# Kernel optimization log

Hardware: AMD Instinct MI355X
Metric: run time of the kernel (lower is better)

## Reference

```python
import jax, jax.numpy as jnp
import numpy as np

DIM = 1024
HEADS = 16
HEAD_DIM = DIM // HEADS
SCALE = HEAD_DIM ** -0.5
B, N = 2, 2048


def setup_inputs() -> dict:
    key = jax.random.key(0)
    ks = jax.random.split(key, 12)
    s = DIM ** -0.5
    return {
        "x_real": jax.random.normal(ks[0], (B, N, DIM), jnp.float32),
        "x_imag": jax.random.normal(ks[1], (B, N, DIM), jnp.float32),
        "Wqkv_r": jax.random.normal(ks[2], (3 * DIM, DIM), jnp.float32) * s,
        "bqkv_r": jax.random.normal(ks[3], (3 * DIM,), jnp.float32) * 0.01,
        "Wqkv_i": jax.random.normal(ks[4], (3 * DIM, DIM), jnp.float32) * s,
        "bqkv_i": jax.random.normal(ks[5], (3 * DIM,), jnp.float32) * 0.01,
        "Wout_r": jax.random.normal(ks[6], (DIM, DIM), jnp.float32) * s,
        "bout_r": jax.random.normal(ks[7], (DIM,), jnp.float32) * 0.01,
        "Wout_i": jax.random.normal(ks[8], (DIM, DIM), jnp.float32) * s,
        "bout_i": jax.random.normal(ks[9], (DIM,), jnp.float32) * 0.01,
    }


def _split_heads(qkv):
    # (B, N, 3*D) -> q, k, v each (B, H, N, hd)
    b, n, _ = qkv.shape
    qkv = qkv.reshape(b, n, 3, HEADS, HEAD_DIM).transpose(2, 0, 3, 1, 4)
    return qkv[0], qkv[1], qkv[2]


def reference(x_real, x_imag, Wqkv_r, bqkv_r, Wqkv_i, bqkv_i,
              Wout_r, bout_r, Wout_i, bout_i):
    b, n, d = x_real.shape
    q_r, k_r, v_r = _split_heads(x_real @ Wqkv_r.T + bqkv_r)
    q_i, k_i, v_i = _split_heads(x_imag @ Wqkv_i.T + bqkv_i)

    # complex score: (q_r + i q_i) (k_r - i k_i)^T pattern per source
    attn_real = (jnp.einsum('bhqd,bhkd->bhqk', q_r, k_r)
                 + jnp.einsum('bhqd,bhkd->bhqk', q_i, k_i)) * SCALE
    attn_imag = (jnp.einsum('bhqd,bhkd->bhqk', q_i, k_r)
                 - jnp.einsum('bhqd,bhkd->bhqk', q_r, k_i)) * SCALE
    attn_mag = jnp.sqrt(attn_real ** 2 + attn_imag ** 2)
    w = jax.nn.softmax(attn_mag, axis=-1)

    out_r = jnp.einsum('bhqk,bhkd->bhqd', w, v_r).transpose(0, 2, 1, 3).reshape(b, n, d)
    out_i = jnp.einsum('bhqk,bhkd->bhqd', w, v_i).transpose(0, 2, 1, 3).reshape(b, n, d)
    out_r = out_r @ Wout_r.T + bout_r
    out_i = out_i @ Wout_i.T + bout_i
    return out_r, out_i
```

## Files before the change

### kernel.cpp

```cpp
#include <hip/hip_runtime.h>


#define DIM_   1024
#define HEADS_ 16
#define HD_    64
#define BB_    2
#define NN_    2048
#define MTOT_  (BB_*NN_)
#define SCALE_ 0.125f
#define QSCALE_ 0.1803368801111243f

typedef __bf16 bf16;
typedef __bf16 bf16x8 __attribute__((ext_vector_type(8)));
typedef short  s16x8  __attribute__((ext_vector_type(8)));
typedef float  fx4    __attribute__((ext_vector_type(4)));

__device__ __forceinline__ bf16x8 neg8(bf16x8 v) {
    s16x8 s;
    __builtin_memcpy(&s, &v, sizeof(s));
    s ^= (short)0x8000;
    bf16x8 r;
    __builtin_memcpy(&r, &s, sizeof(r));
    return r;
}

__device__ __forceinline__ void gl_lds16(const void* g, void* l) {
    __builtin_amdgcn_global_load_lds(
        (const __attribute__((address_space(1))) unsigned int*)g,
        (__attribute__((address_space(3))) unsigned int*)l, 16, 0, 0);
}

#define PIPE_SYNC() asm volatile("s_waitcnt vmcnt(2)\n\ts_barrier" ::: "memory")
#define FULL_SYNC() asm volatile("s_waitcnt vmcnt(0)\n\ts_barrier" ::: "memory")

__global__ __launch_bounds__(256) void cvt_prepass(
    const float* __restrict__ xr, const float* __restrict__ xi,
    const float* __restrict__ wqr, const float* __restrict__ wqi,
    const float* __restrict__ wor, const float* __restrict__ woi,
    bf16* __restrict__ xbf, bf16* __restrict__ wqkv, bf16* __restrict__ wout)
{
    const int bid = blockIdx.x;
    const float* src; bf16* dst; int rel;
    if      (bid < 2048) { src = xr;  dst = xbf;           rel = bid; }
    else if (bid < 4096) { src = xi;  dst = xbf + 4194304; rel = bid - 2048; }
    else if (bid < 5632) { src = wqr; dst = wqkv;          rel = bid - 4096; }
    else if (bid < 7168) { src = wqi; dst = wqkv + 3145728; rel = bid - 5632; }
    else if (bid < 7680) { src = wor; dst = wout;          rel = bid - 7168; }
    else                 { src = woi; dst = wout + 1048576; rel = bid - 7680; }
    size_t base = (size_t)rel * 2048 + (size_t)threadIdx.x * 8;
    fx4 a = *(const fx4*)(src + base);
    fx4 b = *(const fx4*)(src + base + 4);
    bf16x8 o;
#pragma unroll
    for (int j = 0; j < 4; ++j) { o[j] = (bf16)a[j]; o[j+4] = (bf16)b[j]; }
    *(bf16x8*)(dst + base) = o;
}

#define GEMM_CORE(Aptr, Bptr)                                                  \
    __shared__ __align__(16) bf16 As[128*64];                                  \
    __shared__ __align__(16) bf16 Bs[128*64];                                  \
    const int tid  = threadIdx.x;                                              \
    const int w    = tid >> 6, lane = tid & 63;                                \
    const int quad = lane >> 4, lc = lane & 15;                                \
    const int wm   = (w >> 1) * 64, wn = (w & 1) * 64;                         \
    const int rj   = lane >> 3;                                                \
    const int sc   = (lane & 7) ^ rj;                                          \
    const fx4 fzero = {0.f, 0.f, 0.f, 0.f};                                    \
    fx4 acc[4][4];                                                             \
    _Pragma("unroll")                                                          \
    for (int mi = 0; mi < 4; ++mi)                                             \
        _Pragma("unroll")                                                      \
        for (int ni = 0; ni < 4; ++ni) acc[mi][ni] = fzero;                    \
    for (int k0 = 0; k0 < DIM_; k0 += 64) {                                    \
        _Pragma("unroll")                                                      \
        for (int j = 0; j < 4; ++j) {                                          \
            int grp = j*4 + w;                                                 \
            int gr  = grp*8 + rj;                                              \
            gl_lds16(Aptr + (size_t)(m0+gr)*DIM_ + k0 + sc*8, As + grp*512);   \
            gl_lds16(Bptr + (size_t)(n0+gr)*DIM_ + k0 + sc*8, Bs + grp*512);   \
        }                                                                      \
        __syncthreads();                                                       \
        bf16x8 af[2][4], bfr[2][4];                                            \
        _Pragma("unroll")                                                      \
        for (int ks = 0; ks < 2; ++ks) {                                       \
            _Pragma("unroll")                                                  \
            for (int mi = 0; mi < 4; ++mi)                                     \
                af[ks][mi] = *(bf16x8*)&As[(wm+mi*16+lc)*64 + (((ks*4+quad)^(lc&7))*8)]; \
            _Pragma("unroll")                                                  \
            for (int ni = 0; ni < 4; ++ni)                                     \
                bfr[ks][ni] = *(bf16x8*)&Bs[(wn+ni*16+lc)*64 + (((ks*4+quad)^(lc&7))*8)]; \
        }                                                                      \
        _Pragma("unroll")                                                      \
        for (int ks = 0; ks < 2; ++ks)                                         \
            _Pragma("unroll")                                                  \
            for (int mi = 0; mi < 4; ++mi)                                     \
                _Pragma("unroll")                                              \
                for (int ni = 0; ni < 4; ++ni)                                 \
                    acc[mi][ni] = __builtin_amdgcn_mfma_f32_16x16x32_bf16(     \
                        af[ks][mi], bfr[ks][ni], acc[mi][ni], 0, 0, 0);        \
        __syncthreads();                                                       \
    }

__global__ __launch_bounds__(256) void qkv_gemm_dma(
    const bf16* __restrict__ xbf, const bf16* __restrict__ wqkv,
    const float* __restrict__ br, const float* __restrict__ bi,
    bf16* __restrict__ qbuf, bf16* __restrict__ kbuf, bf16* __restrict__ vbuf)
{
    const int z = blockIdx.z;
    const bf16* __restrict__ Ap = xbf  + (size_t)z * 4194304;
    const bf16* __restrict__ Bp = wqkv + (size_t)z * 3145728;
    const float* __restrict__ bias = z ? bi : br;
    const int n0 = blockIdx.x * 128;
    const int m0 = blockIdx.y * 128;

    GEMM_CORE(Ap, Bp)

#pragma unroll
    for (int mi = 0; mi < 4; ++mi)
#pragma unroll
        for (int ni = 0; ni < 4; ++ni)
#pragma unroll
            for (int r = 0; r < 4; ++r) {
                int gm = m0 + wm + mi*16 + quad*4 + r;
                int gc = n0 + wn + ni*16 + lc;
                float val = acc[mi][ni][r] + bias[gc];
                int which = gc >> 10, h = (gc >> 6) & 15, hd = gc & 63;
                if (which == 0) val *= QSCALE_;
                bf16 bv = (bf16)val;
                int b = gm >> 11, n = gm & 2047;
                size_t base = (size_t)((z*BB_ + b)*HEADS_ + h);
                if (which == 0)      qbuf[(base*NN_ + n)*HD_ + hd] = bv;
                else if (which == 1) kbuf[(base*NN_ + n)*HD_ + hd] = bv;
                else                 vbuf[(base*HD_ + hd)*NN_ + n] = bv;
            }
}

__global__ __launch_bounds__(256) void out_gemm_dma(
    const bf16* __restrict__ obuf, const bf16* __restrict__ wout,
    const float* __restrict__ br, const float* __restrict__ bi,
    float* __restrict__ out)
{
    const int z = blockIdx.z;
    const bf16* __restrict__ Ap = obuf + (size_t)z * 4194304;
    const bf16* __restrict__ Bp = wout + (size_t)z * 1048576;
    const float* __restrict__ bias = z ? bi : br;
    float* __restrict__ dst = out + (size_t)z * 4194304;
    const int n0 = blockIdx.x * 128;
    const int m0 = blockIdx.y * 128;

    GEMM_CORE(Ap, Bp)

#pragma unroll
    for (int mi = 0; mi < 4; ++mi)
#pragma unroll
        for (int ni = 0; ni < 4; ++ni)
#pragma unroll
            for (int r = 0; r < 4; ++r) {
                int gm = m0 + wm + mi*16 + quad*4 + r;
                int gc = n0 + wn + ni*16 + lc;
                dst[(size_t)gm*DIM_ + gc] = acc[mi][ni][r] + bias[gc];
            }
}

#define KT 32
#define NSTEP (NN_/KT)

__global__ __launch_bounds__(512, 4) void attn_fwd(
    const bf16* __restrict__ qbuf, const bf16* __restrict__ kbuf,
    const bf16* __restrict__ vbuf, bf16* __restrict__ obuf)
{
    const int bid = blockIdx.x;
    const int xcd = bid & 7;
    const int loc = bid >> 3;
    const int hb  = xcd*4 + (loc >> 4);
    const int blk = loc & 15;
    const int b = hb >> 4, h = hb & 15;

    const int tid  = threadIdx.x;
    const int w    = tid >> 6, lane = tid & 63;
    const int quad = lane >> 4, lc = lane & 15;
    const int q0   = blk*128 + w*16;

    __shared__ __align__(16) bf16 KV[3*8192];

    const size_t hR = (size_t)(b)*HEADS_ + h;
    const size_t hI = (size_t)(BB_ + b)*HEADS_ + h;
    const bf16* qrg = qbuf + hR*NN_*HD_;
    const bf16* qig = qbuf + hI*NN_*HD_;
    const char* krg = (const char*)(kbuf + hR*NN_*HD_);
    const char* kig = (const char*)(kbuf + hI*NN_*HD_);
    const char* vrg = (const char*)(vbuf + hR*HD_*NN_);
    const char* vig = (const char*)(vbuf + hI*HD_*NN_);

    const bf16* pr = qrg + (size_t)(q0 + lc)*HD_ + quad*8;
    const bf16* pi = qig + (size_t)(q0 + lc)*HD_ + quad*8;
    bf16x8 qr0 = *(const bf16x8*)(pr);
    bf16x8 qr1 = *(const bf16x8*)(pr + 32);
    bf16x8 qi0 = *(const bf16x8*)(pi);
    bf16x8 qi1 = *(const bf16x8*)(pi + 32);
    bf16x8 nqr0 = neg8(qr0), nqr1 = neg8(qr1);

    bf16x8 ones;
#pragma unroll
    for (int j = 0; j < 8; ++j) ones[j] = (bf16)1.0f;

    const int arr = w >> 1, half = w & 1;
    const char* stg_base = (arr == 0) ? krg : (arr == 1) ? kig
                         : (arr == 2) ? vrg : vig;
    size_t lane_off, step_mul, j_mul;
    if (arr < 2) {
        const int rl = lane >> 3;
        const int p0 = (rl >> 2)*8 + half*4 + (rl & 3);
        lane_off = (size_t)p0*128 + (size_t)((lane & 7) ^ rl)*16;
        step_mul = 4096;  j_mul = 2048;
    } else {
        lane_off = (size_t)half*131072
                 + (size_t)(lane >> 2)*4096 + (size_t)((lane & 3) ^ ((lane >> 3) & 3))*16;
        step_mul = 64;    j_mul = 65536;
    }
    const char* stg0 = stg_base + lane_off;
    const int lds_base = arr*2048 + half*1024;

    int koff[2][2], voff[4];
#pragma unroll
    for (int kb = 0; kb < 2; ++kb)
#pragma unroll
        for (int hf = 0; hf < 2; ++hf) {
            int r = kb*16 + lc;
            koff[kb][hf] = r*64 + (((hf*4 + quad) ^ (r & 7))*8);
        }
#pragma unroll
    for (int vb = 0; vb < 4; ++vb) {
        int r = vb*16 + lc;
        voff[vb] = r*32 + ((quad ^ ((r >> 1) & 3))*8);
    }

    const fx4 fzero = {0.f, 0.f, 0.f, 0.f};
    fx4 O[2][4];
    fx4 lacc = fzero;
#pragma unroll
    for (int ri = 0; ri < 2; ++ri)
#pragma unroll
        for (int vb = 0; vb < 4; ++vb) O[ri][vb] = fzero;
    bf16x8 pf = {};
    bf16x8 vf[2][4];

    {
        bf16* l = KV + lds_base;
        gl_lds16(stg0,          l);
        gl_lds16(stg0 + j_mul,  l + 512);
        l = KV + 8192 + lds_base;
        gl_lds16(stg0 + step_mul,         l);
        gl_lds16(stg0 + step_mul + j_mul, l + 512);
    }
    PIPE_SYNC();

    int b0 = 0, b1 = 8192, b2 = 16384;
    for (int s = 0; s < NSTEP; ++s) {
        if (s < NSTEP-2) {
            const char* g = stg0 + (size_t)(s+2)*step_mul;
            bf16* l = KV + b2 + lds_base;
            gl_lds16(g,         l);
            gl_lds16(g + j_mul, l + 512);
        }

        if (s > 0) {
            __builtin_amdgcn_s_setprio(1);
#pragma unroll
            for (int ri = 0; ri < 2; ++ri)
#pragma unroll
                for (int vb = 0; vb < 4; ++vb)
                    O[ri][vb] = __builtin_amdgcn_mfma_f32_16x16x32_bf16(
                        pf, vf[ri][vb], O[ri][vb], 0, 0, 0);
            __builtin_amdgcn_s_setprio(0);
        }

        bf16x8 kr_[2][2], ki_[2][2];
#pragma unroll
        for (int kb = 0; kb < 2; ++kb)
#pragma unroll
            for (int hf = 0; hf < 2; ++hf) {
                kr_[kb][hf] = *(bf16x8*)&KV[b0 + koff[kb][hf]];
                ki_[kb][hf] = *(bf16x8*)&KV[b0 + 2048 + koff[kb][hf]];
            }

#pragma unroll
        for (int kb = 0; kb < 2; ++kb) {
            fx4 sr = fzero, si = fzero;
            __builtin_amdgcn_s_setprio(1);
            sr = __builtin_amdgcn_mfma_f32_16x16x32_bf16(kr_[kb][0], qr0,  sr, 0,0,0);
            sr = __builtin_amdgcn_mfma_f32_16x16x32_bf16(kr_[kb][1], qr1,  sr, 0,0,0);
            sr = __builtin_amdgcn_mfma_f32_16x16x32_bf16(ki_[kb][0], qi0,  sr, 0,0,0);
            sr = __builtin_amdgcn_mfma_f32_16x16x32_bf16(ki_[kb][1], qi1,  sr, 0,0,0);
            si = __builtin_amdgcn_mfma_f32_16x16x32_bf16(kr_[kb][0], qi0,  si, 0,0,0);
            si = __builtin_amdgcn_mfma_f32_16x16x32_bf16(kr_[kb][1], qi1,  si, 0,0,0);
            si = __builtin_amdgcn_mfma_f32_16x16x32_bf16(ki_[kb][0], nqr0, si, 0,0,0);
            si = __builtin_amdgcn_mfma_f32_16x16x32_bf16(ki_[kb][1], nqr1, si, 0,0,0);
            __builtin_amdgcn_s_setprio(0);
#pragma unroll
            for (int r4 = 0; r4 < 4; ++r4) {
                float s2 = sr[r4]*sr[r4] + si[r4]*si[r4];
                float mg = __builtin_amdgcn_sqrtf(s2);
                float pv = __builtin_amdgcn_exp2f(mg);
                pf[kb*4 + r4] = (bf16)pv;
            }
        }

        lacc = __builtin_amdgcn_mfma_f32_16x16x32_bf16(pf, ones, lacc, 0, 0, 0);

#pragma unroll
        for (int ri = 0; ri < 2; ++ri)
#pragma unroll
            for (int vb = 0; vb < 4; ++vb)
                vf[ri][vb] = *(bf16x8*)&KV[b0 + (2+ri)*2048 + voff[vb]];

        if (s == NSTEP-2) FULL_SYNC();
        else              PIPE_SYNC();
        int t = b0; b0 = b1; b1 = b2; b2 = t;
    }

    __builtin_amdgcn_s_setprio(1);
#pragma unroll
    for (int ri = 0; ri < 2; ++ri)
#pragma unroll
        for (int vb = 0; vb < 4; ++vb)
            O[ri][vb] = __builtin_amdgcn_mfma_f32_16x16x32_bf16(
                pf, vf[ri][vb], O[ri][vb], 0, 0, 0);
    __builtin_amdgcn_s_setprio(0);

    float inv[4];
#pragma unroll
    for (int r = 0; r < 4; ++r) inv[r] = 1.f / lacc[r];

    bf16* obr = obuf + ((size_t)(b)*NN_)*DIM_;
    bf16* obi = obuf + ((size_t)(BB_ + b)*NN_)*DIM_;
#pragma unroll
    for (int vb = 0; vb < 4; ++vb)
#pragma unroll
        for (int r = 0; r < 4; ++r) {
            int gn = q0 + quad*4 + r;
            int gc = h*HD_ + vb*16 + lc;
            obr[(size_t)gn*DIM_ + gc] = (bf16)(O[0][vb][r] * inv[r]);
            obi[(size_t)gn*DIM_ + gc] = (bf16)(O[1][vb][r] * inv[r]);
        }
}

__global__ __launch_bounds__(256) void qkv_gemm_legacy(
    const float* __restrict__ xr, const float* __restrict__ xi,
    const float* __restrict__ Wr, const float* __restrict__ Wi,
    const float* __restrict__ br, const float* __restrict__ bi,
    bf16* __restrict__ qbuf, bf16* __restrict__ kbuf, bf16* __restrict__ vbuf)
{
    const int z = blockIdx.z;
    const float* __restrict__ A    = z ? xi : xr;
    const float* __restrict__ W    = z ? Wi : Wr;
    const float* __restrict__ bias = z ? bi : br;
    const int n0 = blockIdx.x * 128;
    const int m0 = blockIdx.y * 128;

    __shared__ bf16 As[128*40];
    __shared__ bf16 Bs[128*40];

    const int tid  = threadIdx.x;
    const int w    = tid >> 6, lane = tid & 63;
    const int quad = lane >> 4, lc = lane & 15;
    const int wm   = (w >> 1) * 64, wn = (w & 1) * 64;

    const fx4 fzero = {0.f, 0.f, 0.f, 0.f};
    fx4 acc[4][4];
#pragma unroll
    for (int mi = 0; mi < 4; ++mi)
#pragma unroll
        for (int ni = 0; ni < 4; ++ni) acc[mi][ni] = fzero;

    for (int k0 = 0; k0 < DIM_; k0 += 32) {
#pragma unroll
        for (int it = 0; it < 2; ++it) {
            int flat = it*2048 + tid*8;
            int row = flat >> 5, col = flat & 31;
            const float* pa = A + (size_t)(m0+row)*DIM_ + k0 + col;
            const float* pb = W + (size_t)(n0+row)*DIM_ + k0 + col;
            fx4 a0 = *(const fx4*)pa, a1 = *(const fx4*)(pa+4);
            fx4 b0 = *(const fx4*)pb, b1 = *(const fx4*)(pb+4);
            bf16x8 av, bv;
#pragma unroll
            for (int j = 0; j < 4; ++j) {
                av[j] = (bf16)a0[j]; av[j+4] = (bf16)a1[j];
                bv[j] = (bf16)b0[j]; bv[j+4] = (bf16)b1[j];
            }
            *(bf16x8*)&As[row*40 + col] = av;
            *(bf16x8*)&Bs[row*40 + col] = bv;
        }
        __syncthreads();

        bf16x8 af[4], bfr[4];
#pragma unroll
        for (int mi = 0; mi < 4; ++mi) af[mi]  = *(bf16x8*)&As[(wm + mi*16 + lc)*40 + quad*8];
#pragma unroll
        for (int ni = 0; ni < 4; ++ni) bfr[ni] = *(bf16x8*)&Bs[(wn + ni*16 + lc)*40 + quad*8];
#pragma unroll
        for (int mi = 0; mi < 4; ++mi)
#pragma unroll
            for (int ni = 0; ni < 4; ++ni)
                acc[mi][ni] = __builtin_amdgcn_mfma_f32_16x16x32_bf16(af[mi], bfr[ni], acc[mi][ni], 0, 0, 0);
        __syncthreads();
    }

#pragma unroll
    for (int mi = 0; mi < 4; ++mi)
#pragma unroll
        for (int ni = 0; ni < 4; ++ni)
#pragma unroll
            for (int r = 0; r < 4; ++r) {
                int gm = m0 + wm + mi*16 + quad*4 + r;
                int gc = n0 + wn + ni*16 + lc;
                float val = acc[mi][ni][r] + bias[gc];
                int which = gc >> 10, h = (gc >> 6) & 15, hd = gc & 63;
                if (which == 0) val *= QSCALE_;
                bf16 bv = (bf16)val;
                int b = gm >> 11, n = gm & 2047;
                size_t base = (size_t)((z*BB_ + b)*HEADS_ + h);
                if (which == 0)      qbuf[(base*NN_ + n)*HD_ + hd] = bv;
                else if (which == 1) kbuf[(base*NN_ + n)*HD_ + hd] = bv;
                else                 vbuf[(base*HD_ + hd)*NN_ + n] = bv;
            }
}

__global__ __launch_bounds__(256) void out_gemm_legacy(
    const bf16* __restrict__ obuf,
    const float* __restrict__ Wr, const float* __restrict__ Wi,
    const float* __restrict__ br, const float* __restrict__ bi,
    float* __restrict__ out)
{
    const int z = blockIdx.z;
    const bf16*  __restrict__ A    = obuf + (size_t)z * MTOT_ * DIM_;
    const float* __restrict__ W    = z ? Wi : Wr;
    const float* __restrict__ bias = z ? bi : br;
    float* __restrict__ dst        = out + (size_t)z * MTOT_ * DIM_;
    const int n0 = blockIdx.x * 128;
    const int m0 = blockIdx.y * 128;

    __shared__ bf16 As[128*40];
    __shared__ bf16 Bs[128*40];

    const int tid  = threadIdx.x;
    const int w    = tid >> 6, lane = tid & 63;
    const int quad = lane >> 4, lc = lane & 15;
    const int wm   = (w >> 1) * 64, wn = (w & 1) * 64;

    const fx4 fzero = {0.f, 0.f, 0.f, 0.f};
    fx4 acc[4][4];
#pragma unroll
    for (int mi = 0; mi < 4; ++mi)
#pragma unroll
        for (int ni = 0; ni < 4; ++ni) acc[mi][ni] = fzero;

    for (int k0 = 0; k0 < DIM_; k0 += 32) {
#pragma unroll
        for (int it = 0; it < 2; ++it) {
            int flat = it*2048 + tid*8;
            int row = flat >> 5, col = flat & 31;
            *(bf16x8*)&As[row*40 + col] = *(const bf16x8*)(A + (size_t)(m0+row)*DIM_ + k0 + col);
            const float* pb = W + (size_t)(n0+row)*DIM_ + k0 + col;
            fx4 b0 = *(const fx4*)pb, b1 = *(const fx4*)(pb+4);
            bf16x8 bv;
#pragma unroll
            for (int j = 0; j < 4; ++j) { bv[j] = (bf16)b0[j]; bv[j+4] = (bf16)b1[j]; }
            *(bf16x8*)&Bs[row*40 + col] = bv;
        }
        __syncthreads();

        bf16x8 af[4], bfr[4];
#pragma unroll
        for (int mi = 0; mi < 4; ++mi) af[mi]  = *(bf16x8*)&As[(wm + mi*16 + lc)*40 + quad*8];
#pragma unroll
        for (int ni = 0; ni < 4; ++ni) bfr[ni] = *(bf16x8*)&Bs[(wn + ni*16 + lc)*40 + quad*8];
#pragma unroll
        for (int mi = 0; mi < 4; ++mi)
#pragma unroll
            for (int ni = 0; ni < 4; ++ni)
                acc[mi][ni] = __builtin_amdgcn_mfma_f32_16x16x32_bf16(af[mi], bfr[ni], acc[mi][ni], 0, 0, 0);
        __syncthreads();
    }

#pragma unroll
    for (int mi = 0; mi < 4; ++mi)
#pragma unroll
        for (int ni = 0; ni < 4; ++ni)
#pragma unroll
            for (int r = 0; r < 4; ++r) {
                int gm = m0 + wm + mi*16 + quad*4 + r;
                int gc = n0 + wn + ni*16 + lc;
                dst[(size_t)gm*DIM_ + gc] = acc[mi][ni][r] + bias[gc];
            }
}

extern "C" void kernel_launch(void* const* d_in, const int* in_sizes, int n_in,
                              void* d_out, int out_size, void* d_ws, size_t ws_size,
                              hipStream_t stream) {
    const float* xr  = (const float*)d_in[0];
    const float* xi  = (const float*)d_in[1];
    const float* Wqr = (const float*)d_in[2];
    const float* bqr = (const float*)d_in[3];
    const float* Wqi = (const float*)d_in[4];
    const float* bqi = (const float*)d_in[5];
    const float* Wor = (const float*)d_in[6];
    const float* bor = (const float*)d_in[7];
    const float* Woi = (const float*)d_in[8];
    const float* boi = (const float*)d_in[9];
    float* out = (float*)d_out;

    bf16* ws = (bf16*)d_ws;
    const size_t NEED = 83886080ull;

    if (ws_size >= NEED) {
        bf16* xbf  = ws;
        bf16* wqkv = ws + 8388608;
        bf16* wout = ws + 14680064;
        bf16* qb   = ws + 16777216;
        bf16* kb   = ws + 25165824;
        bf16* vb   = ws + 33554432;
        bf16* obuf = xbf;

        cvt_prepass<<<dim3(8192), 256, 0, stream>>>(xr, xi, Wqr, Wqi, Wor, Woi,
                                                    xbf, wqkv, wout);
        qkv_gemm_dma<<<dim3(24, 32, 2), 256, 0, stream>>>(xbf, wqkv, bqr, bqi,
                                                          qb, kb, vb);
        attn_fwd<<<dim3(512), 512, 0, stream>>>(qb, kb, vb, obuf);
        out_gemm_dma<<<dim3(8, 32, 2), 256, 0, stream>>>(obuf, wout, bor, boi, out);
    } else {
        const size_t per = (size_t)2 * BB_ * HEADS_ * NN_ * HD_;
        bf16* qb   = ws;
        bf16* kb   = ws + per;
        bf16* vb   = ws + 2*per;
        bf16* obuf = ws + 3*per;
        qkv_gemm_legacy<<<dim3(24, 32, 2), 256, 0, stream>>>(xr, xi, Wqr, Wqi,
                                                             bqr, bqi, qb, kb, vb);
        attn_fwd<<<dim3(512), 512, 0, stream>>>(qb, kb, vb, obuf);
        out_gemm_legacy<<<dim3(8, 32, 2), 256, 0, stream>>>(obuf, Wor, Woi,
                                                            bor, boi, out);
    }
}
```

Before: 340.5 us.

## Process two KV tiles per barrier with double-buffered pair staging

Restructures the attention main loop so that each iteration handles two KV tiles and waits on a single full barrier, using four LDS buffers arranged as two ping-pong pairs instead of a three-buffer ring with a barrier per tile. The intent is to halve the number of barriers and waitcnts in the hot loop. In exchange, LDS use per block grows from 48KB to 64KB, which may reduce the number of resident blocks per CU. The barrier now waits for all outstanding loads (vmcnt(0)), so prefetch of the next pair is exposed at each sync.

After: 343.9 us. Within noise of the previous version (+1.0%).

```diff
diff --git a/kernel.cpp b/kernel.cpp
--- a/kernel.cpp
+++ b/kernel.cpp
@@ -30,7 +30,6 @@
         (__attribute__((address_space(3))) unsigned int*)l, 16, 0, 0);
 }
 
-#define PIPE_SYNC() asm volatile("s_waitcnt vmcnt(2)\n\ts_barrier" ::: "memory")
 #define FULL_SYNC() asm volatile("s_waitcnt vmcnt(0)\n\ts_barrier" ::: "memory")
 
 __global__ __launch_bounds__(256) void cvt_prepass(
@@ -181,7 +180,7 @@
     const int quad = lane >> 4, lc = lane & 15;
     const int q0   = blk*128 + w*16;
 
-    __shared__ __align__(16) bf16 KV[3*8192];
+    __shared__ __align__(16) bf16 KV[4*8192];
 
     const size_t hR = (size_t)(b)*HEADS_ + h;
     const size_t hI = (size_t)(BB_ + b)*HEADS_ + h;
@@ -242,48 +241,35 @@
     for (int ri = 0; ri < 2; ++ri)
 #pragma unroll
         for (int vb = 0; vb < 4; ++vb) O[ri][vb] = fzero;
-    bf16x8 pf = {};
+    bf16x8 pfp = {}, pf0 = {}, pf1 = {};
     bf16x8 vf[2][4];
 
-    {
-        bf16* l = KV + lds_base;
-        gl_lds16(stg0,          l);
-        gl_lds16(stg0 + j_mul,  l + 512);
-        l = KV + 8192 + lds_base;
-        gl_lds16(stg0 + step_mul,         l);
-        gl_lds16(stg0 + step_mul + j_mul, l + 512);
-    }
-    PIPE_SYNC();
-
-    int b0 = 0, b1 = 8192, b2 = 16384;
-    for (int s = 0; s < NSTEP; ++s) {
-        if (s < NSTEP-2) {
-            const char* g = stg0 + (size_t)(s+2)*step_mul;
-            bf16* l = KV + b2 + lds_base;
-            gl_lds16(g,         l);
-            gl_lds16(g + j_mul, l + 512);
-        }
-
-        if (s > 0) {
-            __builtin_amdgcn_s_setprio(1);
-#pragma unroll
-            for (int ri = 0; ri < 2; ++ri)
-#pragma unroll
-                for (int vb = 0; vb < 4; ++vb)
-                    O[ri][vb] = __builtin_amdgcn_mfma_f32_16x16x32_bf16(
-                        pf, vf[ri][vb], O[ri][vb], 0, 0, 0);
-            __builtin_amdgcn_s_setprio(0);
-        }
-
+    auto PVSTEP = [&](bf16x8 pf) {
+        __builtin_amdgcn_s_setprio(1);
+#pragma unroll
+        for (int ri = 0; ri < 2; ++ri)
+#pragma unroll
+            for (int vb = 0; vb < 4; ++vb)
+                O[ri][vb] = __builtin_amdgcn_mfma_f32_16x16x32_bf16(
+                    pf, vf[ri][vb], O[ri][vb], 0, 0, 0);
+        __builtin_amdgcn_s_setprio(0);
+    };
+    auto VREAD = [&](int c) {
+#pragma unroll
+        for (int ri = 0; ri < 2; ++ri)
+#pragma unroll
+            for (int vb = 0; vb < 4; ++vb)
+                vf[ri][vb] = *(bf16x8*)&KV[c + (2+ri)*2048 + voff[vb]];
+    };
+    auto TILE = [&](int c, bf16x8& pfo) {
         bf16x8 kr_[2][2], ki_[2][2];
 #pragma unroll
         for (int kb = 0; kb < 2; ++kb)
 #pragma unroll
             for (int hf = 0; hf < 2; ++hf) {
-                kr_[kb][hf] = *(bf16x8*)&KV[b0 + koff[kb][hf]];
-                ki_[kb][hf] = *(bf16x8*)&KV[b0 + 2048 + koff[kb][hf]];
-            }
-
+                kr_[kb][hf] = *(bf16x8*)&KV[c + koff[kb][hf]];
+                ki_[kb][hf] = *(bf16x8*)&KV[c + 2048 + koff[kb][hf]];
+            }
 #pragma unroll
         for (int kb = 0; kb < 2; ++kb) {
             fx4 sr = fzero, si = fzero;
@@ -302,31 +288,51 @@
                 float s2 = sr[r4]*sr[r4] + si[r4]*si[r4];
                 float mg = __builtin_amdgcn_sqrtf(s2);
                 float pv = __builtin_amdgcn_exp2f(mg);
-                pf[kb*4 + r4] = (bf16)pv;
+                pfo[kb*4 + r4] = (bf16)pv;
             }
         }
-
-        lacc = __builtin_amdgcn_mfma_f32_16x16x32_bf16(pf, ones, lacc, 0, 0, 0);
-
-#pragma unroll
-        for (int ri = 0; ri < 2; ++ri)
-#pragma unroll
-            for (int vb = 0; vb < 4; ++vb)
-                vf[ri][vb] = *(bf16x8*)&KV[b0 + (2+ri)*2048 + voff[vb]];
-
-        if (s == NSTEP-2) FULL_SYNC();
-        else              PIPE_SYNC();
-        int t = b0; b0 = b1; b1 = b2; b2 = t;
-    }
-
-    __builtin_amdgcn_s_setprio(1);
-#pragma unroll
-    for (int ri = 0; ri < 2; ++ri)
-#pragma unroll
-        for (int vb = 0; vb < 4; ++vb)
-            O[ri][vb] = __builtin_amdgcn_mfma_f32_16x16x32_bf16(
-                pf, vf[ri][vb], O[ri][vb], 0, 0, 0);
-    __builtin_amdgcn_s_setprio(0);
+        lacc = __builtin_amdgcn_mfma_f32_16x16x32_bf16(pfo, ones, lacc, 0, 0, 0);
+    };
+
+    {
+        bf16* l0 = KV + lds_base;
+        gl_lds16(stg0,          l0);
+        gl_lds16(stg0 + j_mul,  l0 + 512);
+        bf16* l1 = KV + 8192 + lds_base;
+        gl_lds16(stg0 + step_mul,         l1);
+        gl_lds16(stg0 + step_mul + j_mul, l1 + 512);
+    }
+    FULL_SYNC();
+
+    for (int T = 0; T < NSTEP/2; ++T) {
+        const int c0 = (T & 1) ? 16384 : 0;
+        const int c1 = c0 + 8192;
+
+        if (T < NSTEP/2 - 1) {
+            const char* g0 = stg0 + (size_t)(2*T+2)*step_mul;
+            bf16* l0 = KV + (c0 ^ 16384) + lds_base;
+            gl_lds16(g0,         l0);
+            gl_lds16(g0 + j_mul, l0 + 512);
+            const char* g1 = stg0 + (size_t)(2*T+3)*step_mul;
+            bf16* l1 = KV + (c1 ^ 16384) + lds_base;
+            gl_lds16(g1,         l1);
+            gl_lds16(g1 + j_mul, l1 + 512);
+        }
+
+        if (T > 0) PVSTEP(pfp);
+
+        TILE(c0, pf0);
+        VREAD(c0);
+        PVSTEP(pf0);
+
+        TILE(c1, pf1);
+        VREAD(c1);
+        pfp = pf1;
+
+        FULL_SYNC();
+    }
+
+    PVSTEP(pfp);
 
     float inv[4];
 #pragma unroll
```
